# Performance work log

Measured on AMD Instinct MI355X. Metric: run time of the kernel, lower is better.

Reference implementation:

```python
import jax, jax.numpy as jnp
import numpy as np
from jax import lax

D_MODEL = 1024
D_STATE = 16
D_CONV = 4
EXPAND = 2
D_INNER = D_MODEL * EXPAND
B, T = 2, 1024


def setup_inputs() -> dict:
    key = jax.random.key(0)
    ks = jax.random.split(key, 8)
    s = 0.02
    x = jax.random.normal(ks[0], (B, T, D_MODEL), dtype=jnp.float32)
    in_proj_w = jax.random.normal(ks[1], (D_MODEL, 2 * D_INNER), dtype=jnp.float32) * s
    conv_w = jax.random.normal(ks[2], (D_INNER, 1, D_CONV), dtype=jnp.float32) * s  # depthwise [O, I/G=1, K]
    conv_b = jax.random.normal(ks[3], (D_INNER,), dtype=jnp.float32) * s
    x_proj_w = jax.random.normal(ks[4], (D_INNER, 2 * D_STATE + 1), dtype=jnp.float32) * s
    dt_proj_w = jax.random.normal(ks[5], (1, D_INNER), dtype=jnp.float32) * s
    dt_proj_b = jax.random.normal(ks[6], (D_INNER,), dtype=jnp.float32) * s
    # Canonical Mamba init: A_log = log(1..d_state) broadcast over d_inner
    A_log = jnp.broadcast_to(jnp.log(jnp.arange(1, D_STATE + 1, dtype=jnp.float32))[None, :], (D_INNER, D_STATE))
    D_param = jnp.ones((D_INNER,), dtype=jnp.float32)
    c_proj_w = jax.random.normal(ks[7], (D_INNER, D_MODEL), dtype=jnp.float32) * s
    return {"x": x, "in_proj_w": in_proj_w, "conv_w": conv_w, "conv_b": conv_b,
            "x_proj_w": x_proj_w, "dt_proj_w": dt_proj_w, "dt_proj_b": dt_proj_b,
            "A_log": A_log, "D_param": D_param, "c_proj_w": c_proj_w}


def _mamba_fwd(x, in_proj_w, conv_w, conv_b, x_proj_w, dt_proj_w, dt_proj_b, A_log, D_param, c_proj_w):
    Bb, Tt, _ = x.shape
    xz = jnp.einsum('btd,de->bte', x, in_proj_w)          # [B,T,2*Di]
    x_branch, z = jnp.split(xz, 2, axis=-1)               # [B,T,Di] each
    # Causal depthwise conv1d: pad left K-1 (== torch pad both + slice[:T])
    xb = jnp.transpose(x_branch, (0, 2, 1))               # [B,Di,T]
    xb = lax.conv_general_dilated(xb, conv_w, window_strides=(1,),
                                  padding=[(D_CONV - 1, 0)],
                                  feature_group_count=D_INNER,
                                  dimension_numbers=('NCH', 'OIH', 'NCH'))
    xb = xb + conv_b[None, :, None]
    x_branch = jax.nn.silu(jnp.transpose(xb, (0, 2, 1)))  # [B,T,Di]
    x_ssm = jnp.einsum('btd,dk->btk', x_branch, x_proj_w) # [B,T,2S+1]
    B_t = x_ssm[:, :, :D_STATE]                            # [B,T,S]
    C_t = x_ssm[:, :, D_STATE:2 * D_STATE]                 # [B,T,S]
    dt = x_ssm[:, :, -1:]                                  # [B,T,1]
    dt = jax.nn.softplus(jnp.einsum('btk,kd->btd', dt, dt_proj_w) + dt_proj_b)  # [B,T,Di]
    A = -jnp.exp(A_log)                                    # [Di,S]
    A_bar = jnp.exp(dt[..., None] * A[None, None])         # [B,T,Di,S]
    Bx = (dt[..., None] * B_t[:, :, None, :]) * x_branch[..., None]  # [B,T,Di,S]

    def step(h, inp):
        a, bx, c = inp                                     # [B,Di,S],[B,Di,S],[B,S]
        h = a * h + bx
        y = jnp.einsum('bds,bs->bd', h, c)
        return h, y

    h0 = jnp.zeros((Bb, D_INNER, D_STATE), dtype=x.dtype)
    _, ys = lax.scan(step, h0,
                     (jnp.transpose(A_bar, (1, 0, 2, 3)),
                      jnp.transpose(Bx, (1, 0, 2, 3)),
                      jnp.transpose(C_t, (1, 0, 2))))
    y = jnp.transpose(ys, (1, 0, 2))                       # [B,T,Di]
    y = y + D_param[None, None, :] * x_branch
    y = y * jax.nn.silu(z)
    return jnp.einsum('btd,de->bte', y, c_proj_w)          # [B,T,d_model]


def reference(x, in_proj_w, conv_w, conv_b, x_proj_w, dt_proj_w, dt_proj_b, A_log, D_param, c_proj_w):
    return _mamba_fwd(x, in_proj_w, conv_w, conv_b, x_proj_w, dt_proj_w, dt_proj_b, A_log, D_param, c_proj_w)
```

## Files before the change

### kernel.cpp

```cpp
#include <hip/hip_runtime.h>
#include <math.h>

#define DMODEL 1024
#define DSTATE 16
#define DCONV 4
#define DINNER 2048
#define BATCH 2
#define SEQ 1024
#define BT (BATCH*SEQ)
#define NC 32
#define LC 32

typedef unsigned short ushort_t;
typedef __attribute__((ext_vector_type(8))) short short8;
typedef __attribute__((ext_vector_type(4))) float f32x4;

__device__ __forceinline__ ushort_t f2bf(float f) {
    union { float f; unsigned int u; } v; v.f = f;
    unsigned int r = v.u + 0x7fffu + ((v.u >> 16) & 1u);
    return (ushort_t)(r >> 16);
}
__device__ __forceinline__ float bf2f(ushort_t u) {
    union { unsigned int u; float f; } v; v.u = ((unsigned int)u) << 16;
    return v.f;
}
__device__ __forceinline__ float softplusf(float x) {
    return (x > 20.f) ? x : log1pf(__expf(x));
}

#define GLOAD_LDS16(G, L) \
  __builtin_amdgcn_global_load_lds((const __attribute__((address_space(1))) void*)(G), \
                                   (__attribute__((address_space(3))) void*)(L), 16, 0, 0)

__global__ __launch_bounds__(256) void prep_kernel(const float* __restrict__ x,
                                                   ushort_t* __restrict__ xbf,
                                                   const float* __restrict__ w1,
                                                   ushort_t* __restrict__ w1T,
                                                   const float* __restrict__ w2,
                                                   ushort_t* __restrict__ w2T,
                                                   const float* __restrict__ wx,
                                                   ushort_t* __restrict__ wT,
                                                   float* __restrict__ zacc)
{
    __shared__ float t[32][33];
    const int bid = blockIdx.x;
    const int tid = threadIdx.x;

    if (bid < 1024) {
        size_t i = ((size_t)bid * 256 + tid) * 8;
        float4 a = *(const float4*)&x[i];
        float4 b = *(const float4*)&x[i + 4];
        uint4 p;
        p.x = (unsigned)f2bf(a.x) | ((unsigned)f2bf(a.y) << 16);
        p.y = (unsigned)f2bf(a.z) | ((unsigned)f2bf(a.w) << 16);
        p.z = (unsigned)f2bf(b.x) | ((unsigned)f2bf(b.y) << 16);
        p.w = (unsigned)f2bf(b.z) | ((unsigned)f2bf(b.w) << 16);
        *(uint4*)&xbf[i] = p;
        if (bid < 66) {
            size_t z = ((size_t)bid * 256 + tid) * 4;
            *(float4*)&zacc[z] = make_float4(0.f, 0.f, 0.f, 0.f);
        }
        return;
    }

    if (bid >= 7168) {
        __shared__ ushort_t th[32][48];
        __shared__ ushort_t tl[32][48];
        const int r0 = (bid - 7168) * 32;
        for (int e = tid; e < 32 * 48; e += 256) {
            int k = e / 48, n = e % 48;
            float v = (n < 33) ? wx[(size_t)(r0 + k) * 33 + n] : 0.f;
            ushort_t hi = f2bf(v);
            th[k][n] = hi;
            tl[k][n] = f2bf(v - bf2f(hi));
        }
        __syncthreads();
        for (int e = tid; e < 48 * 32; e += 256) {
            int n = e >> 5, k = e & 31;
            wT[(size_t)n * DINNER + r0 + k]        = th[k][n];
            wT[(size_t)(48 + n) * DINNER + r0 + k] = tl[k][n];
        }
        return;
    }

    const float* in; ushort_t* out; int R, Cc, r0, c0;
    if (bid < 5120) {
        int b2 = bid - 1024;
        in = w1; out = w1T; R = DMODEL; Cc = 2 * DINNER;
        r0 = (b2 >> 7) * 32; c0 = (b2 & 127) * 32;
    } else {
        int b3 = bid - 5120;
        in = w2; out = w2T; R = DINNER; Cc = DMODEL;
        r0 = (b3 >> 5) * 32; c0 = (b3 & 31) * 32;
    }
    {
        int lr = tid >> 3, lc4 = (tid & 7) * 4;
        float4 v = *(const float4*)&in[(size_t)(r0 + lr) * Cc + c0 + lc4];
        t[lr][lc4 + 0] = v.x; t[lr][lc4 + 1] = v.y;
        t[lr][lc4 + 2] = v.z; t[lr][lc4 + 3] = v.w;
    }
    __syncthreads();
    {
        int oc = tid >> 3, rq = (tid & 7) * 4;
        ushort4 u;
        u.x = f2bf(t[rq + 0][oc]);
        u.y = f2bf(t[rq + 1][oc]);
        u.z = f2bf(t[rq + 2][oc]);
        u.w = f2bf(t[rq + 3][oc]);
        *(ushort4*)&out[(size_t)(c0 + oc) * R + r0 + rq] = u;
    }
}

__global__ __launch_bounds__(256) void gemm_in(const ushort_t* __restrict__ A,
                                               const ushort_t* __restrict__ Bt,
                                               ushort_t* __restrict__ xzb,
                                               ushort_t* __restrict__ zsil)
{
    constexpr int BM = 128, BN = 128, BK = 64;
    constexpr int AL = BM * BK / (256 * 8);
    constexpr int BL = BN * BK / (256 * 8);
    constexpr int FM = BM / 32;
    constexpr int FN = BN / 32;
    const int K = DMODEL;
    __shared__ __align__(16) ushort_t Al[BM * BK];
    __shared__ __align__(16) ushort_t Bl[BN * BK];

    const int tid  = threadIdx.x;
    const int lane = tid & 63;
    const int wid  = tid >> 6;
    const int wr   = wid >> 1;
    const int wc   = wid & 1;
    const int bm   = blockIdx.y * BM;
    const int bn   = blockIdx.x * BN;

    f32x4 acc[FM][FN] = {};

    for (int k0 = 0; k0 < K; k0 += BK) {
#pragma unroll
        for (int j = 0; j < AL; j++) {
            int chunk = j * 256 + tid;
            GLOAD_LDS16(&A[(size_t)(bm + (chunk >> 3)) * K + k0 + (chunk & 7) * 8],
                        &Al[(size_t)(j * 256 + wid * 64) * 8]);
        }
#pragma unroll
        for (int j = 0; j < BL; j++) {
            int chunk = j * 256 + tid;
            GLOAD_LDS16(&Bt[(size_t)(bn + (chunk >> 3)) * K + k0 + (chunk & 7) * 8],
                        &Bl[(size_t)(j * 256 + wid * 64) * 8]);
        }
        __syncthreads();

#pragma unroll
        for (int kk = 0; kk < 2; kk++) {
            short8 af[FM], bf[FN];
#pragma unroll
            for (int m = 0; m < FM; m++)
                af[m] = *(const short8*)&Al[(wr * (BM / 2) + m * 16 + (lane & 15)) * BK
                                            + (lane >> 4) * 8 + kk * 32];
#pragma unroll
            for (int n = 0; n < FN; n++)
                bf[n] = *(const short8*)&Bl[(wc * (BN / 2) + n * 16 + (lane & 15)) * BK
                                            + (lane >> 4) * 8 + kk * 32];
#pragma unroll
            for (int m = 0; m < FM; m++)
#pragma unroll
                for (int n = 0; n < FN; n++)
                    acc[m][n] = __builtin_amdgcn_mfma_f32_16x16x32_bf16(af[m], bf[n], acc[m][n], 0, 0, 0);
        }
        __syncthreads();
    }

    if (bn < DINNER) {
#pragma unroll
        for (int m = 0; m < FM; m++)
#pragma unroll
            for (int n = 0; n < FN; n++) {
                int row0 = bm + wr * (BM / 2) + m * 16 + (lane >> 4) * 4;
                int col  = bn + wc * (BN / 2) + n * 16 + (lane & 15);
#pragma unroll
                for (int r = 0; r < 4; r++)
                    xzb[(size_t)(row0 + r) * DINNER + col] = f2bf(acc[m][n][r]);
            }
    } else {
#pragma unroll
        for (int m = 0; m < FM; m++)
#pragma unroll
            for (int n = 0; n < FN; n++) {
                int row0 = bm + wr * (BM / 2) + m * 16 + (lane >> 4) * 4;
                int col  = bn - DINNER + wc * (BN / 2) + n * 16 + (lane & 15);
#pragma unroll
                for (int r = 0; r < 4; r++) {
                    float z = acc[m][n][r];
                    zsil[(size_t)(row0 + r) * DINNER + col] = f2bf(z / (1.f + __expf(-z)));
                }
            }
    }
}

__global__ __launch_bounds__(256) void gemm_out(const ushort_t* __restrict__ A,
                                                const ushort_t* __restrict__ Bt,
                                                float* __restrict__ C)
{
    constexpr int BM = 64, BN = 64, BK = 64;
    constexpr int AL = BM * BK / (256 * 8);
    constexpr int BL = BN * BK / (256 * 8);
    constexpr int FM = BM / 32;
    constexpr int FN = BN / 32;
    const int N = DMODEL, K = DINNER;
    __shared__ __align__(16) ushort_t Al[BM * BK];
    __shared__ __align__(16) ushort_t Bl[BN * BK];

    const int tid  = threadIdx.x;
    const int lane = tid & 63;
    const int wid  = tid >> 6;
    const int wr   = wid >> 1;
    const int wc   = wid & 1;
    const int bm   = blockIdx.y * BM;
    const int bn   = blockIdx.x * BN;

    f32x4 acc[FM][FN] = {};

    for (int k0 = 0; k0 < K; k0 += BK) {
#pragma unroll
        for (int j = 0; j < AL; j++) {
            int chunk = j * 256 + tid;
            GLOAD_LDS16(&A[(size_t)(bm + (chunk >> 3)) * K + k0 + (chunk & 7) * 8],
                        &Al[(size_t)(j * 256 + wid * 64) * 8]);
        }
#pragma unroll
        for (int j = 0; j < BL; j++) {
            int chunk = j * 256 + tid;
            GLOAD_LDS16(&Bt[(size_t)(bn + (chunk >> 3)) * K + k0 + (chunk & 7) * 8],
                        &Bl[(size_t)(j * 256 + wid * 64) * 8]);
        }
        __syncthreads();

#pragma unroll
        for (int kk = 0; kk < 2; kk++) {
            short8 af[FM], bf[FN];
#pragma unroll
            for (int m = 0; m < FM; m++)
                af[m] = *(const short8*)&Al[(wr * (BM / 2) + m * 16 + (lane & 15)) * BK
                                            + (lane >> 4) * 8 + kk * 32];
#pragma unroll
            for (int n = 0; n < FN; n++)
                bf[n] = *(const short8*)&Bl[(wc * (BN / 2) + n * 16 + (lane & 15)) * BK
                                            + (lane >> 4) * 8 + kk * 32];
#pragma unroll
            for (int m = 0; m < FM; m++)
#pragma unroll
                for (int n = 0; n < FN; n++)
                    acc[m][n] = __builtin_amdgcn_mfma_f32_16x16x32_bf16(af[m], bf[n], acc[m][n], 0, 0, 0);
        }
        __syncthreads();
    }

#pragma unroll
    for (int m = 0; m < FM; m++)
#pragma unroll
        for (int n = 0; n < FN; n++) {
            int row0 = bm + wr * (BM / 2) + m * 16 + (lane >> 4) * 4;
            int col  = bn + wc * (BN / 2) + n * 16 + (lane & 15);
#pragma unroll
            for (int r = 0; r < 4; r++)
                C[(size_t)(row0 + r) * N + col] = acc[m][n][r];
        }
}

__global__ __launch_bounds__(256) void xproj_mfma(const ushort_t* __restrict__ A,
                                                  const ushort_t* __restrict__ wT,
                                                  float* __restrict__ Btb,
                                                  float* __restrict__ Ctb,
                                                  float* __restrict__ dtraw)
{
    constexpr int BK = 64;
    __shared__ __align__(16) ushort_t Al[64 * BK];
    __shared__ __align__(16) ushort_t Bl[96 * BK];

    const int tid  = threadIdx.x;
    const int lane = tid & 63;
    const int wid  = tid >> 6;
    const int kc   = blockIdx.x * 256;
    const int bm   = blockIdx.y * 64;

    f32x4 acc[6] = {};

    for (int ks = 0; ks < 4; ks++) {
        const int kbase = kc + ks * BK;
#pragma unroll
        for (int j = 0; j < 2; j++) {
            int chunk = j * 256 + tid;
            GLOAD_LDS16(&A[(size_t)(bm + (chunk >> 3)) * DINNER + kbase + (chunk & 7) * 8],
                        &Al[(size_t)(j * 256 + wid * 64) * 8]);
        }
#pragma unroll
        for (int j = 0; j < 3; j++) {
            int chunk = j * 256 + tid;
            GLOAD_LDS16(&wT[(size_t)(chunk >> 3) * DINNER + kbase + (chunk & 7) * 8],
                        &Bl[(size_t)(j * 256 + wid * 64) * 8]);
        }
        __syncthreads();

#pragma unroll
        for (int kk = 0; kk < 2; kk++) {
            short8 af = *(const short8*)&Al[(wid * 16 + (lane & 15)) * BK
                                            + (lane >> 4) * 8 + kk * 32];
#pragma unroll
            for (int n = 0; n < 6; n++) {
                short8 bf = *(const short8*)&Bl[(n * 16 + (lane & 15)) * BK
                                                + (lane >> 4) * 8 + kk * 32];
                acc[n] = __builtin_amdgcn_mfma_f32_16x16x32_bf16(af, bf, acc[n], 0, 0, 0);
            }
        }
        __syncthreads();
    }

    const int n   = lane & 15;
    const int row = bm + wid * 16 + (lane >> 4) * 4;
#pragma unroll
    for (int nf = 0; nf < 3; nf++) {
        f32x4 v = acc[nf] + acc[nf + 3];
        int ng = nf * 16 + n;
        if (ng < 16) {
#pragma unroll
            for (int r = 0; r < 4; r++)
                atomicAdd(&Btb[(size_t)(row + r) * 16 + ng], v[r]);
        } else if (ng < 32) {
#pragma unroll
            for (int r = 0; r < 4; r++)
                atomicAdd(&Ctb[(size_t)(row + r) * 16 + (ng - 16)], v[r]);
        } else if (ng == 32) {
#pragma unroll
            for (int r = 0; r < 4; r++)
                atomicAdd(&dtraw[row + r], v[r]);
        }
    }
}

__global__ __launch_bounds__(256) void conv_silu_kernel(const ushort_t* __restrict__ xzb,
                                                        const float* __restrict__ cw,
                                                        const float* __restrict__ cb,
                                                        ushort_t* __restrict__ xbb)
{
    __shared__ float tile[64 + 3][64];
    const int b  = blockIdx.z;
    const int t0 = blockIdx.x * 64;
    const int d0 = blockIdx.y * 64;
    const int tid = threadIdx.x;

    for (int e = tid; e < 67 * 8; e += 256) {
        int r  = e >> 3;
        int c8 = (e & 7) * 8;
        int t  = t0 - 3 + r;
        if (t >= 0) {
            short8 v = *(const short8*)&xzb[((size_t)b * SEQ + t) * DINNER + d0 + c8];
#pragma unroll
            for (int k = 0; k < 8; k++)
                tile[r][c8 + k] = bf2f((ushort_t)v[k]);
        } else {
#pragma unroll
            for (int k = 0; k < 8; k++)
                tile[r][c8 + k] = 0.f;
        }
    }
    __syncthreads();

    const int dl = tid & 63;
    const int tb = tid >> 6;
    const int d  = d0 + dl;
    const float w0 = cw[d * 4 + 0], w1 = cw[d * 4 + 1];
    const float w2 = cw[d * 4 + 2], w3 = cw[d * 4 + 3];
    const float bias = cb[d];

#pragma unroll
    for (int ii = 0; ii < 16; ii++) {
        int tl = tb + 4 * ii;
        float s = bias;
        s = fmaf(tile[tl + 0][dl], w0, s);
        s = fmaf(tile[tl + 1][dl], w1, s);
        s = fmaf(tile[tl + 2][dl], w2, s);
        s = fmaf(tile[tl + 3][dl], w3, s);
        float sil = s / (1.f + __expf(-s));
        xbb[((size_t)b * SEQ + t0 + tl) * DINNER + d] = f2bf(sil);
    }
}

__device__ __forceinline__ void qpowers(float q, float* a)
{
    float q2 = q * q, q4 = q2 * q2, q8 = q4 * q4;
    a[0] = q;        a[1] = q2;       a[2] = q2 * q;   a[3] = q4;
    a[4] = q4 * q;   a[5] = q4 * q2;  a[6] = q4 * a[2];a[7] = q8;
    a[8] = q8 * q;   a[9] = q8 * q2;  a[10]= q8 * a[2];a[11]= q8 * q4;
    a[12]= q8 * a[4];a[13]= q8 * a[5];a[14]= q8 * a[6];a[15]= q8 * q8;
}

__device__ __forceinline__ bool a_structure_ok(const float* A_log, int d, float As2_0)
{
    bool ok = true;
#pragma unroll
    for (int s = 1; s < 16; s++) {
        float v = -__expf(A_log[d * 16 + s]) * 1.44269504f;
        ok &= (fabsf(v - (float)(s + 1) * As2_0) <= 1e-4f * (float)(s + 1) * fabsf(As2_0));
    }
    return ok;
}

__device__ __forceinline__ void stage_xs(const ushort_t* __restrict__ xbb,
                                         float (*xs)[256],
                                         int b, int t0, int d0, int tid)
{
#pragma unroll
    for (int j = 0; j < 4; j++) {
        int e = j * 256 + tid;
        int rr = e >> 5, cc8 = (e & 31) * 8;
        short8 v = *(const short8*)&xbb[((size_t)b * SEQ + t0 + rr) * DINNER + d0 + cc8];
#pragma unroll
        for (int k = 0; k < 8; k++)
            xs[rr][cc8 + k] = bf2f((ushort_t)v[k]);
    }
}

__global__ __launch_bounds__(256) void scan1_kernel(const ushort_t* __restrict__ xbb,
                                                    const float* __restrict__ dtraw,
                                                    const float* __restrict__ Btb,
                                                    const float* __restrict__ A_log,
                                                    const float* __restrict__ dtw,
                                                    const float* __restrict__ dtb,
                                                    float* __restrict__ Hend,
                                                    float* __restrict__ dtsum)
{
    __shared__ float raw[LC];
    __shared__ float xs[LC][256];
    __shared__ float Bs[LC][16];

    const int tid = threadIdx.x;
    const int c   = blockIdx.x;
    const int b   = blockIdx.z;
    const int d0  = blockIdx.y * 256;
    const int d   = d0 + tid;
    const int t0  = c * LC;

    if (tid < LC / 4)
        *(float4*)&raw[tid * 4] = *(const float4*)&dtraw[b * SEQ + t0 + tid * 4];
    if (tid < 128)
        *(float4*)&Bs[0][tid * 4] = *(const float4*)&Btb[((size_t)b * SEQ + t0) * 16 + tid * 4];
    stage_xs(xbb, xs, b, t0, d0, tid);

    const float wd = dtw[d], bd = dtb[d];
    const float As2_0 = -__expf(A_log[d * 16]) * 1.44269504f;
    const bool fast = a_structure_ok(A_log, d, As2_0);

    float h[16];
#pragma unroll
    for (int s = 0; s < 16; s++) h[s] = 0.f;
    float dsum = 0.f;
    __syncthreads();

    if (fast) {
#pragma unroll 2
        for (int t = 0; t < LC; t++) {
            float dt = softplusf(fmaf(raw[t], wd, bd));
            float xv = xs[t][tid];
            float Bv[16];
#pragma unroll
            for (int s4 = 0; s4 < 4; s4++)
                *(float4*)&Bv[s4 * 4] = *(const float4*)&Bs[t][s4 * 4];
            float a[16];
            qpowers(exp2f(dt * As2_0), a);
            float dtx = dt * xv;
            dsum += dt;
#pragma unroll
            for (int s = 0; s < 16; s++)
                h[s] = fmaf(a[s], h[s], Bv[s] * dtx);
        }
    } else {
        float As2[16];
#pragma unroll
        for (int s = 0; s < 16; s++)
            As2[s] = -__expf(A_log[d * 16 + s]) * 1.44269504f;
#pragma unroll 2
        for (int t = 0; t < LC; t++) {
            float dt = softplusf(fmaf(raw[t], wd, bd));
            float xv = xs[t][tid];
            float Bv[16];
#pragma unroll
            for (int s4 = 0; s4 < 4; s4++)
                *(float4*)&Bv[s4 * 4] = *(const float4*)&Bs[t][s4 * 4];
            float dtx = dt * xv;
            dsum += dt;
#pragma unroll
            for (int s = 0; s < 16; s++)
                h[s] = fmaf(exp2f(dt * As2[s]), h[s], Bv[s] * dtx);
        }
    }

    size_t hb = (((size_t)b * NC + c) * DINNER + d) * 16;
#pragma unroll
    for (int s4 = 0; s4 < 4; s4++)
        *(float4*)&Hend[hb + s4 * 4] = *(float4*)&h[s4 * 4];
    dtsum[((size_t)b * NC + c) * DINNER + d] = dsum;
}

__global__ __launch_bounds__(256) void carry_kernel(const float* __restrict__ Hend,
                                                    const float* __restrict__ dtsum,
                                                    const float* __restrict__ A_log,
                                                    float* __restrict__ Hstart)
{
    const int idx = blockIdx.x * 256 + threadIdx.x;
    const int s = idx & 15;
    const int d = (idx >> 4) & (DINNER - 1);
    const int b = idx >> 15;
    const float As2 = -__expf(A_log[d * 16 + s]) * 1.44269504f;
    float hs = 0.f;
    for (int c = 0; c < NC; c++) {
        size_t off = ((size_t)b * NC + c);
        float P  = exp2f(As2 * dtsum[off * DINNER + d]);
        size_t hi = (off * DINNER + d) * 16 + s;
        float he = Hend[hi];
        Hstart[hi] = hs;
        hs = fmaf(P, hs, he);
    }
}

__global__ __launch_bounds__(256) void scan3_kernel(const ushort_t* __restrict__ xbb,
                                                    const float* __restrict__ dtraw,
                                                    const float* __restrict__ Btb,
                                                    const float* __restrict__ Ctb,
                                                    const float* __restrict__ A_log,
                                                    const float* __restrict__ dtw,
                                                    const float* __restrict__ dtb,
                                                    const float* __restrict__ Hstart,
                                                    const ushort_t* __restrict__ zsil,
                                                    const float* __restrict__ Dp,
                                                    ushort_t* __restrict__ ygb)
{
    __shared__ float raw[LC];
    __shared__ float xs[LC][256];
    __shared__ float Bs[LC][16];
    __shared__ float Cs[LC][16];

    const int tid = threadIdx.x;
    const int c   = blockIdx.x;
    const int b   = blockIdx.z;
    const int d0  = blockIdx.y * 256;
    const int d   = d0 + tid;
    const int t0  = c * LC;

    if (tid < LC / 4)
        *(float4*)&raw[tid * 4] = *(const float4*)&dtraw[b * SEQ + t0 + tid * 4];
    if (tid < 128)
        *(float4*)&Bs[0][tid * 4] = *(const float4*)&Btb[((size_t)b * SEQ + t0) * 16 + tid * 4];
    else {
        int u = tid - 128;
        *(float4*)&Cs[0][u * 4] = *(const float4*)&Ctb[((size_t)b * SEQ + t0) * 16 + u * 4];
    }
    stage_xs(xbb, xs, b, t0, d0, tid);

    const float wd = dtw[d], bd = dtb[d];
    const float Dd = Dp[d];
    const float As2_0 = -__expf(A_log[d * 16]) * 1.44269504f;
    const bool fast = a_structure_ok(A_log, d, As2_0);

    float h[16];
    {
        size_t hb = (((size_t)b * NC + c) * DINNER + d) * 16;
#pragma unroll
        for (int s4 = 0; s4 < 4; s4++)
            *(float4*)&h[s4 * 4] = *(const float4*)&Hstart[hb + s4 * 4];
    }
    __syncthreads();

    if (fast) {
#pragma unroll 2
        for (int t = 0; t < LC; t++) {
            float dt = softplusf(fmaf(raw[t], wd, bd));
            float xv = xs[t][tid];
            float Bv[16], Cv[16];
#pragma unroll
            for (int s4 = 0; s4 < 4; s4++) {
                *(float4*)&Bv[s4 * 4] = *(const float4*)&Bs[t][s4 * 4];
                *(float4*)&Cv[s4 * 4] = *(const float4*)&Cs[t][s4 * 4];
            }
            float a[16];
            qpowers(exp2f(dt * As2_0), a);
            float dtx = dt * xv;
            float acc = 0.f;
#pragma unroll
            for (int s = 0; s < 16; s++) {
                h[s] = fmaf(a[s], h[s], Bv[s] * dtx);
                acc = fmaf(h[s], Cv[s], acc);
            }
            xs[t][tid] = fmaf(Dd, xv, acc);
        }
    } else {
        float As2[16];
#pragma unroll
        for (int s = 0; s < 16; s++)
            As2[s] = -__expf(A_log[d * 16 + s]) * 1.44269504f;
#pragma unroll 2
        for (int t = 0; t < LC; t++) {
            float dt = softplusf(fmaf(raw[t], wd, bd));
            float xv = xs[t][tid];
            float Bv[16], Cv[16];
#pragma unroll
            for (int s4 = 0; s4 < 4; s4++) {
                *(float4*)&Bv[s4 * 4] = *(const float4*)&Bs[t][s4 * 4];
                *(float4*)&Cv[s4 * 4] = *(const float4*)&Cs[t][s4 * 4];
            }
            float dtx = dt * xv;
            float acc = 0.f;
#pragma unroll
            for (int s = 0; s < 16; s++) {
                h[s] = fmaf(exp2f(dt * As2[s]), h[s], Bv[s] * dtx);
                acc = fmaf(h[s], Cv[s], acc);
            }
            xs[t][tid] = fmaf(Dd, xv, acc);
        }
    }
    __syncthreads();

#pragma unroll
    for (int j = 0; j < 8; j++) {
        int e = j * 256 + tid;
        int rr = e >> 6, c4 = (e & 63) * 4;
        float4 yv = *(const float4*)&xs[rr][c4];
        ushort4 zv = *(const ushort4*)&zsil[((size_t)b * SEQ + t0 + rr) * DINNER + d0 + c4];
        ushort4 u;
        u.x = f2bf(yv.x * bf2f(zv.x));
        u.y = f2bf(yv.y * bf2f(zv.y));
        u.z = f2bf(yv.z * bf2f(zv.z));
        u.w = f2bf(yv.w * bf2f(zv.w));
        *(ushort4*)&ygb[((size_t)b * SEQ + t0 + rr) * DINNER + d0 + c4] = u;
    }
}

extern "C" void kernel_launch(void* const* d_in, const int* in_sizes, int n_in,
                              void* d_out, int out_size, void* d_ws, size_t ws_size,
                              hipStream_t stream)
{
    const float* x         = (const float*)d_in[0];
    const float* in_proj_w = (const float*)d_in[1];
    const float* conv_w    = (const float*)d_in[2];
    const float* conv_b    = (const float*)d_in[3];
    const float* x_proj_w  = (const float*)d_in[4];
    const float* dt_proj_w = (const float*)d_in[5];
    const float* dt_proj_b = (const float*)d_in[6];
    const float* A_log     = (const float*)d_in[7];
    const float* D_param   = (const float*)d_in[8];
    const float* c_proj_w  = (const float*)d_in[9];
    float* out = (float*)d_out;

    float* ws    = (float*)d_ws;
    float* Btb   = ws;
    float* Ctb   = Btb + (size_t)BT * 16;
    float* dtraw = Ctb + (size_t)BT * 16;
    float* Hend  = dtraw + BT;
    float* Hstart= Hend + (size_t)BATCH * NC * DINNER * 16;
    float* dtsum = Hstart + (size_t)BATCH * NC * DINNER * 16;
    ushort_t* xbf  = (ushort_t*)(dtsum + (size_t)BATCH * NC * DINNER);
    ushort_t* w1T  = xbf + (size_t)BT * DMODEL;
    ushort_t* w2T  = w1T + (size_t)(2 * DINNER) * DMODEL;
    ushort_t* ygb  = w2T + (size_t)DMODEL * DINNER;
    ushort_t* zsil = ygb + (size_t)BT * DINNER;
    ushort_t* xbb  = zsil + (size_t)BT * DINNER;
    ushort_t* xzb  = xbb + (size_t)BT * DINNER;
    ushort_t* wT   = xzb + (size_t)BT * DINNER;

    prep_kernel<<<dim3(1024 + 4096 + 2048 + 64), 256, 0, stream>>>(
        x, xbf, in_proj_w, w1T, c_proj_w, w2T, x_proj_w, wT, Btb);

    gemm_in<<<dim3(32, 16), 256, 0, stream>>>(xbf, w1T, xzb, zsil);

    conv_silu_kernel<<<dim3(SEQ / 64, DINNER / 64, BATCH), 256, 0, stream>>>(
        xzb, conv_w, conv_b, xbb);

    xproj_mfma<<<dim3(8, 32), 256, 0, stream>>>(xbb, wT, Btb, Ctb, dtraw);

    scan1_kernel<<<dim3(NC, DINNER / 256, BATCH), 256, 0, stream>>>(
        xbb, dtraw, Btb, A_log, dt_proj_w, dt_proj_b, Hend, dtsum);
    carry_kernel<<<dim3(BATCH * DINNER * 16 / 256), 256, 0, stream>>>(
        Hend, dtsum, A_log, Hstart);
    scan3_kernel<<<dim3(NC, DINNER / 256, BATCH), 256, 0, stream>>>(
        xbb, dtraw, Btb, Ctb, A_log, dt_proj_w, dt_proj_b, Hstart, zsil, D_param, ygb);

    gemm_out<<<dim3(16, 32), 256, 0, stream>>>(ygb, w2T, out);
}
```

Measured before the change: 142.0 us.

## Fuse causal depthwise conv and SiLU into input projection GEMM epilogue

```diff
diff --git a/kernel.cpp b/kernel.cpp
--- a/kernel.cpp
+++ b/kernel.cpp
@@ -113,17 +113,17 @@
 
 __global__ __launch_bounds__(256) void gemm_in(const ushort_t* __restrict__ A,
                                                const ushort_t* __restrict__ Bt,
-                                               ushort_t* __restrict__ xzb,
+                                               const float* __restrict__ cw,
+                                               const float* __restrict__ cb,
+                                               ushort_t* __restrict__ xbb,
                                                ushort_t* __restrict__ zsil)
 {
     constexpr int BM = 128, BN = 128, BK = 64;
-    constexpr int AL = BM * BK / (256 * 8);
-    constexpr int BL = BN * BK / (256 * 8);
-    constexpr int FM = BM / 32;
-    constexpr int FN = BN / 32;
+    constexpr int FM = 4, FN = 4;
     const int K = DMODEL;
-    __shared__ __align__(16) ushort_t Al[BM * BK];
+    __shared__ __align__(16) ushort_t Al[144 * BK];
     __shared__ __align__(16) ushort_t Bl[BN * BK];
+    __shared__ float cbuf[144][65];
 
     const int tid  = threadIdx.x;
     const int lane = tid & 63;
@@ -132,18 +132,28 @@
     const int wc   = wid & 1;
     const int bm   = blockIdx.y * BM;
     const int bn   = blockIdx.x * BN;
+    const bool isx = (bn < DINNER);
+    const bool bnd = ((bm & 1023) == 0);
 
     f32x4 acc[FM][FN] = {};
+    f32x4 accx[FN] = {};
 
     for (int k0 = 0; k0 < K; k0 += BK) {
 #pragma unroll
-        for (int j = 0; j < AL; j++) {
+        for (int j = 0; j < 4; j++) {
             int chunk = j * 256 + tid;
             GLOAD_LDS16(&A[(size_t)(bm + (chunk >> 3)) * K + k0 + (chunk & 7) * 8],
                         &Al[(size_t)(j * 256 + wid * 64) * 8]);
         }
-#pragma unroll
-        for (int j = 0; j < BL; j++) {
+        if (isx && tid < 128) {
+            int chunk = 1024 + tid;
+            int erow  = (chunk >> 3) - 128;
+            int arow  = bnd ? (bm + erow) : (bm - 16 + erow);
+            GLOAD_LDS16(&A[(size_t)arow * K + k0 + (chunk & 7) * 8],
+                        &Al[(size_t)(1024 + wid * 64) * 8]);
+        }
+#pragma unroll
+        for (int j = 0; j < 4; j++) {
             int chunk = j * 256 + tid;
             GLOAD_LDS16(&Bt[(size_t)(bn + (chunk >> 3)) * K + k0 + (chunk & 7) * 8],
                         &Bl[(size_t)(j * 256 + wid * 64) * 8]);
@@ -155,39 +165,81 @@
             short8 af[FM], bf[FN];
 #pragma unroll
             for (int m = 0; m < FM; m++)
-                af[m] = *(const short8*)&Al[(wr * (BM / 2) + m * 16 + (lane & 15)) * BK
+                af[m] = *(const short8*)&Al[(wr * 64 + m * 16 + (lane & 15)) * BK
                                             + (lane >> 4) * 8 + kk * 32];
 #pragma unroll
             for (int n = 0; n < FN; n++)
-                bf[n] = *(const short8*)&Bl[(wc * (BN / 2) + n * 16 + (lane & 15)) * BK
+                bf[n] = *(const short8*)&Bl[(wc * 64 + n * 16 + (lane & 15)) * BK
                                             + (lane >> 4) * 8 + kk * 32];
 #pragma unroll
             for (int m = 0; m < FM; m++)
 #pragma unroll
                 for (int n = 0; n < FN; n++)
                     acc[m][n] = __builtin_amdgcn_mfma_f32_16x16x32_bf16(af[m], bf[n], acc[m][n], 0, 0, 0);
+            if (isx && wid < 2) {
+                short8 afx = *(const short8*)&Al[(128 + (lane & 15)) * BK
+                                                 + (lane >> 4) * 8 + kk * 32];
+#pragma unroll
+                for (int n = 0; n < FN; n++)
+                    accx[n] = __builtin_amdgcn_mfma_f32_16x16x32_bf16(afx, bf[n], accx[n], 0, 0, 0);
+            }
         }
         __syncthreads();
     }
 
-    if (bn < DINNER) {
+    if (isx) {
+#pragma unroll
+        for (int p = 0; p < 2; p++) {
+            if (wc == p) {
+#pragma unroll
+                for (int m = 0; m < FM; m++)
+#pragma unroll
+                    for (int n = 0; n < FN; n++) {
+                        int cr = 16 + wr * 64 + m * 16 + (lane >> 4) * 4;
+                        int cc = n * 16 + (lane & 15);
+#pragma unroll
+                        for (int r = 0; r < 4; r++)
+                            cbuf[cr + r][cc] = acc[m][n][r];
+                    }
+                if (wid == p) {
+#pragma unroll
+                    for (int n = 0; n < FN; n++) {
+                        int cr = (lane >> 4) * 4;
+                        int cc = n * 16 + (lane & 15);
+#pragma unroll
+                        for (int r = 0; r < 4; r++)
+                            cbuf[cr + r][cc] = bnd ? 0.f : accx[n][r];
+                    }
+                }
+            }
+            __syncthreads();
+            {
+                int dl   = tid & 63, tb2 = tid >> 6;
+                int gcol = bn + p * 64 + dl;
+                float w0 = cw[gcol * 4 + 0], w1 = cw[gcol * 4 + 1];
+                float w2 = cw[gcol * 4 + 2], w3 = cw[gcol * 4 + 3];
+                float bias = cb[gcol];
+#pragma unroll
+                for (int ii = 0; ii < 32; ii++) {
+                    int tr = tb2 + 4 * ii;
+                    float s = bias;
+                    s = fmaf(cbuf[tr + 13][dl], w0, s);
+                    s = fmaf(cbuf[tr + 14][dl], w1, s);
+                    s = fmaf(cbuf[tr + 15][dl], w2, s);
+                    s = fmaf(cbuf[tr + 16][dl], w3, s);
+                    float sil = s / (1.f + __expf(-s));
+                    xbb[(size_t)(bm + tr) * DINNER + gcol] = f2bf(sil);
+                }
+            }
+            __syncthreads();
+        }
+    } else {
 #pragma unroll
         for (int m = 0; m < FM; m++)
 #pragma unroll
             for (int n = 0; n < FN; n++) {
-                int row0 = bm + wr * (BM / 2) + m * 16 + (lane >> 4) * 4;
-                int col  = bn + wc * (BN / 2) + n * 16 + (lane & 15);
-#pragma unroll
-                for (int r = 0; r < 4; r++)
-                    xzb[(size_t)(row0 + r) * DINNER + col] = f2bf(acc[m][n][r]);
-            }
-    } else {
-#pragma unroll
-        for (int m = 0; m < FM; m++)
-#pragma unroll
-            for (int n = 0; n < FN; n++) {
-                int row0 = bm + wr * (BM / 2) + m * 16 + (lane >> 4) * 4;
-                int col  = bn - DINNER + wc * (BN / 2) + n * 16 + (lane & 15);
+                int row0 = bm + wr * 64 + m * 16 + (lane >> 4) * 4;
+                int col  = bn - DINNER + wc * 64 + n * 16 + (lane & 15);
 #pragma unroll
                 for (int r = 0; r < 4; r++) {
                     float z = acc[m][n][r];
@@ -334,54 +386,6 @@
             for (int r = 0; r < 4; r++)
                 atomicAdd(&dtraw[row + r], v[r]);
         }
-    }
-}
-
-__global__ __launch_bounds__(256) void conv_silu_kernel(const ushort_t* __restrict__ xzb,
-                                                        const float* __restrict__ cw,
-                                                        const float* __restrict__ cb,
-                                                        ushort_t* __restrict__ xbb)
-{
-    __shared__ float tile[64 + 3][64];
-    const int b  = blockIdx.z;
-    const int t0 = blockIdx.x * 64;
-    const int d0 = blockIdx.y * 64;
-    const int tid = threadIdx.x;
-
-    for (int e = tid; e < 67 * 8; e += 256) {
-        int r  = e >> 3;
-        int c8 = (e & 7) * 8;
-        int t  = t0 - 3 + r;
-        if (t >= 0) {
-            short8 v = *(const short8*)&xzb[((size_t)b * SEQ + t) * DINNER + d0 + c8];
-#pragma unroll
-            for (int k = 0; k < 8; k++)
-                tile[r][c8 + k] = bf2f((ushort_t)v[k]);
-        } else {
-#pragma unroll
-            for (int k = 0; k < 8; k++)
-                tile[r][c8 + k] = 0.f;
-        }
-    }
-    __syncthreads();
-
-    const int dl = tid & 63;
-    const int tb = tid >> 6;
-    const int d  = d0 + dl;
-    const float w0 = cw[d * 4 + 0], w1 = cw[d * 4 + 1];
-    const float w2 = cw[d * 4 + 2], w3 = cw[d * 4 + 3];
-    const float bias = cb[d];
-
-#pragma unroll
-    for (int ii = 0; ii < 16; ii++) {
-        int tl = tb + 4 * ii;
-        float s = bias;
-        s = fmaf(tile[tl + 0][dl], w0, s);
-        s = fmaf(tile[tl + 1][dl], w1, s);
-        s = fmaf(tile[tl + 2][dl], w2, s);
-        s = fmaf(tile[tl + 3][dl], w3, s);
-        float sil = s / (1.f + __expf(-s));
-        xbb[((size_t)b * SEQ + t0 + tl) * DINNER + d] = f2bf(sil);
     }
 }
 
@@ -663,16 +667,12 @@
     ushort_t* ygb  = w2T + (size_t)DMODEL * DINNER;
     ushort_t* zsil = ygb + (size_t)BT * DINNER;
     ushort_t* xbb  = zsil + (size_t)BT * DINNER;
-    ushort_t* xzb  = xbb + (size_t)BT * DINNER;
-    ushort_t* wT   = xzb + (size_t)BT * DINNER;
+    ushort_t* wT   = xbb + (size_t)BT * DINNER;
 
     prep_kernel<<<dim3(1024 + 4096 + 2048 + 64), 256, 0, stream>>>(
         x, xbf, in_proj_w, w1T, c_proj_w, w2T, x_proj_w, wT, Btb);
 
-    gemm_in<<<dim3(32, 16), 256, 0, stream>>>(xbf, w1T, xzb, zsil);
-
-    conv_silu_kernel<<<dim3(SEQ / 64, DINNER / 64, BATCH), 256, 0, stream>>>(
-        xzb, conv_w, conv_b, xbb);
+    gemm_in<<<dim3(32, 16), 256, 0, stream>>>(xbf, w1T, conv_w, conv_b, xbb, zsil);
 
     xproj_mfma<<<dim3(8, 32), 256, 0, stream>>>(xbb, wT, Btb, Ctb, dtraw);
 
```

Result: slower. 160.0 us (+12.7%).
